# Kernel tuning notes

Hardware: AMD Instinct MI355X
Metric: run time of the kernel (lower is better)

## Reference

```python
import jax, jax.numpy as jnp
import numpy as np
import math

B, T, D, K, KER, H = 2, 2048, 1024, 16, 7, 2048


def _decay_logit_init(k: int, dmin: float = 0.9, dmax: float = 0.999) -> np.ndarray:
    decays = np.exp(np.linspace(math.log(dmin), math.log(dmax), k))
    return (np.log(decays) - np.log1p(-decays)).astype(np.float32)


def setup_inputs() -> dict:
    key = jax.random.key(0)
    ks = jax.random.split(key, 12)
    s = 0.02
    return {
        "x": jax.random.normal(ks[0], (B, T, D), jnp.float32),
        "conv_w": jax.random.normal(ks[1], (D, KER), jnp.float32) * s,   # depthwise causal conv taps
        "gate_w": jax.random.normal(ks[2], (D, D), jnp.float32) * (D ** -0.5),
        "gate_b": jnp.zeros((D,), jnp.float32),
        "up_w": jax.random.normal(ks[3], (D, H), jnp.float32) * (D ** -0.5),
        "up_b": jnp.zeros((H,), jnp.float32),
        "down_w": jax.random.normal(ks[4], (H, D), jnp.float32) * (H ** -0.5),
        "down_b": jnp.zeros((D,), jnp.float32),
        "sin_w": jax.random.normal(ks[5], (D, K * D), jnp.float32) * (D ** -0.5),
        "sout_w": jax.random.normal(ks[6], (K * D, D), jnp.float32) * ((K * D) ** -0.5),
        "decay_logit": jnp.asarray(_decay_logit_init(K)),
        "gl_w": jax.random.normal(ks[7], (D, 1), jnp.float32) * (D ** -0.5),
        "gl_b": jnp.zeros((1,), jnp.float32),
    }


def _rmsnorm(x, eps=1e-6):
    return x * jax.lax.rsqrt(jnp.mean(x * x, axis=-1, keepdims=True) + eps)


def reference(x, conv_w, gate_w, gate_b, up_w, up_b, down_w, down_b,
              sin_w, sout_w, decay_logit, gl_w, gl_b):
    b, t, d = x.shape
    k_taps = conv_w.shape[1]
    nk = decay_logit.shape[0]

    u = _rmsnorm(x)  # (B,T,D)

    # --- local mixer: causal depthwise conv (zero history buffer) + sigmoid gate + SiLU MLP ---
    u_pad = jnp.pad(u, ((0, 0), (k_taps - 1, 0), (0, 0)))
    y = sum(conv_w[:, j] * u_pad[:, j:j + t, :] for j in range(k_taps))  # (B,T,D)
    g = jax.nn.sigmoid(u @ gate_w + gate_b)
    h = y * g
    local = jax.nn.silu(h @ up_w + up_b) @ down_w + down_b

    # --- state bank: K leaky integrators, s_t = a*s_{t-1} + (1-a)*z_t ---
    z = (u @ sin_w).reshape(b, t, nk, d)  # (B,T,K,D)
    a = jax.nn.sigmoid(decay_logit)[:, None]  # (K,1)

    def step(s, z_t):
        s = a * s + (1.0 - a) * z_t
        return s, s

    s0 = jnp.zeros((b, nk, d), x.dtype)
    _, S = jax.lax.scan(step, s0, jnp.swapaxes(z, 0, 1))  # (T,B,K,D)
    S = jnp.swapaxes(S, 0, 1).reshape(b, t, nk * d)
    long_path = S @ sout_w  # (B,T,D)

    # --- gate fusion + residual (memory table is empty at init -> mem term == 0) ---
    g_long = jax.nn.sigmoid(u @ gl_w + gl_b)  # (B,T,1)
    return x + local + g_long * long_path
```

## Files before the change

kernel.cpp:

```cpp
#include <hip/hip_runtime.h>
#include <cstdint>
#include <cstddef>

typedef __attribute__((ext_vector_type(8))) short short8;
typedef __attribute__((ext_vector_type(4))) float floatx4;

#define DEV static __device__ __forceinline__

#define PSTRIDE ((size_t)4096 * 1024)

DEV unsigned short f2bf(float f) {
  union { float f; uint32_t u; } v; v.f = f;
  uint32_t r = v.u + 0x7fffu + ((v.u >> 16) & 1u);
  return (unsigned short)(r >> 16);
}
DEV float bf2f(unsigned short h) {
  union { uint32_t u; float f; } v; v.u = ((uint32_t)h) << 16; return v.f;
}
DEV float sigmoidf_(float x) { return 1.f / (1.f + __expf(-x)); }

DEV void gld_lds16(const unsigned short* g, unsigned short* l) {
  __builtin_amdgcn_global_load_lds(
      (const __attribute__((address_space(1))) void*)g,
      (__attribute__((address_space(3))) void*)l, 16, 0, 0);
}

__global__ __launch_bounds__(256) void transpose_kernel(
    const float* __restrict__ W, unsigned short* __restrict__ Wt,
    int Kdim, int Ndim) {
  __shared__ float tile[32][33];
  const int n0 = blockIdx.x * 32;
  const int k0 = blockIdx.y * 32;
  const int tx = threadIdx.x & 31;
  const int ty = threadIdx.x >> 5;
#pragma unroll
  for (int r = 0; r < 32; r += 8)
    tile[ty + r][tx] = W[(size_t)(k0 + ty + r) * Ndim + n0 + tx];
  __syncthreads();
#pragma unroll
  for (int r = 0; r < 32; r += 8)
    Wt[(size_t)(n0 + ty + r) * Kdim + k0 + tx] = f2bf(tile[tx][ty + r]);
}

__global__ __launch_bounds__(256) void cast_kernel(
    const float* __restrict__ W, unsigned short* __restrict__ Wb) {
  const size_t i = (size_t)blockIdx.x * 256 + threadIdx.x;
  const float4 v = ((const float4*)W)[i];
  ushort4 o;
  o.x = f2bf(v.x); o.y = f2bf(v.y); o.z = f2bf(v.z); o.w = f2bf(v.w);
  ((ushort4*)Wb)[i] = o;
}

__global__ __launch_bounds__(256) void rmsnorm_kernel(
    const float* __restrict__ x, const float* __restrict__ gl_w,
    const float* __restrict__ gl_b, unsigned short* __restrict__ u,
    float* __restrict__ gl_logit) {
  const int row = blockIdx.x;
  const int tid = threadIdx.x;
  const float4 v = ((const float4*)(x + (size_t)row * 1024))[tid];
  float ss = v.x * v.x + v.y * v.y + v.z * v.z + v.w * v.w;
#pragma unroll
  for (int o = 32; o > 0; o >>= 1) ss += __shfl_down(ss, o, 64);
  __shared__ float red[4];
  if ((tid & 63) == 0) red[tid >> 6] = ss;
  __syncthreads();
  const float tot = red[0] + red[1] + red[2] + red[3];
  const float r = rsqrtf(tot * (1.f / 1024.f) + 1e-6f);
  const float ux = v.x * r, uy = v.y * r, uz = v.z * r, uw = v.w * r;
  ushort4 ub;
  ub.x = f2bf(ux); ub.y = f2bf(uy); ub.z = f2bf(uz); ub.w = f2bf(uw);
  ((ushort4*)(u + (size_t)row * 1024))[tid] = ub;
  const float4 w4 = ((const float4*)gl_w)[tid];
  float dot = ux * w4.x + uy * w4.y + uz * w4.z + uw * w4.w;
#pragma unroll
  for (int o = 32; o > 0; o >>= 1) dot += __shfl_down(dot, o, 64);
  __syncthreads();
  if ((tid & 63) == 0) red[tid >> 6] = dot;
  __syncthreads();
  if (tid == 0) gl_logit[row] = red[0] + red[1] + red[2] + red[3] + gl_b[0];
}

template <int EPI>
__global__ __launch_bounds__(256, 2) void gemm_bt(
    const unsigned short* __restrict__ A, const unsigned short* __restrict__ Bt,
    const float* __restrict__ bias, void* __restrict__ Cout, int Ndim, int Kdim) {
  __shared__ unsigned short As[128 * 32];
  __shared__ unsigned short Bs[128 * 32];
  const int tid = threadIdx.x;
  const int wave = tid >> 6;
  const int lane = tid & 63;
  const size_t row0 = (size_t)blockIdx.x * 128;
  const size_t col0 = (size_t)blockIdx.y * 128;

  const int srow = wave * 32 + (lane >> 2);
  const int kofs = (lane & 3) * 8;
  const unsigned short* pA0 = A + (row0 + srow) * (size_t)Kdim + kofs;
  const unsigned short* pA1 = A + (row0 + srow + 16) * (size_t)Kdim + kofs;
  const unsigned short* pB0 = Bt + (col0 + srow) * (size_t)Kdim + kofs;
  const unsigned short* pB1 = Bt + (col0 + srow + 16) * (size_t)Kdim + kofs;
  unsigned short* lA0 = &As[(wave * 2 + 0) * 512];
  unsigned short* lA1 = &As[(wave * 2 + 1) * 512];
  unsigned short* lB0 = &Bs[(wave * 2 + 0) * 512];
  unsigned short* lB1 = &Bs[(wave * 2 + 1) * 512];

  const int wm = (wave & 1) * 64;
  const int wn = (wave >> 1) * 64;
  const int lr = lane & 15;
  const int lq = lane >> 4;
  const int a_off = (wm + lr) * 32 + lq * 8;
  const int b_off = (wn + lr) * 32 + lq * 8;

  floatx4 acc[4][4];
#pragma unroll
  for (int i = 0; i < 4; i++)
#pragma unroll
    for (int j = 0; j < 4; j++) acc[i][j] = floatx4{0.f, 0.f, 0.f, 0.f};

  for (int kt = 0; kt < Kdim; kt += 32) {
    __syncthreads();
    gld_lds16(pA0, lA0);
    gld_lds16(pA1, lA1);
    gld_lds16(pB0, lB0);
    gld_lds16(pB1, lB1);
    pA0 += 32; pA1 += 32; pB0 += 32; pB1 += 32;
    __syncthreads();
    short8 af[4], bfr[4];
#pragma unroll
    for (int i = 0; i < 4; i++) af[i] = *(const short8*)&As[a_off + i * 16 * 32];
#pragma unroll
    for (int j = 0; j < 4; j++) bfr[j] = *(const short8*)&Bs[b_off + j * 16 * 32];
#pragma unroll
    for (int i = 0; i < 4; i++)
#pragma unroll
      for (int j = 0; j < 4; j++)
        acc[i][j] = __builtin_amdgcn_mfma_f32_16x16x32_bf16(af[i], bfr[j], acc[i][j], 0, 0, 0);
  }

#pragma unroll
  for (int i = 0; i < 4; i++) {
    const size_t rbase = row0 + wm + 16 * i + lq * 4;
#pragma unroll
    for (int j = 0; j < 4; j++) {
      const size_t c = col0 + wn + 16 * j + lr;
#pragma unroll
      for (int r = 0; r < 4; r++) {
        float v = acc[i][j][r];
        const size_t off = (rbase + r) * (size_t)Ndim + c;
        if constexpr (EPI == 2) {
          v += bias[c];
          ((unsigned short*)Cout)[off] = f2bf(v * sigmoidf_(v));
        } else {
          ((unsigned short*)Cout)[off] = f2bf(v);
        }
      }
    }
  }
}

__global__ __launch_bounds__(256, 2) void gemm_splitkP(
    const unsigned short* __restrict__ A, const unsigned short* __restrict__ Bt,
    unsigned short* __restrict__ PBase, int Kdim, int splitLen) {
  __shared__ unsigned short As[128 * 32];
  __shared__ unsigned short Bs[128 * 32];
  const int split = blockIdx.z;
  const int k0 = split * splitLen;
  const int klen = min(splitLen, Kdim - k0);
  const int tid = threadIdx.x;
  const int wave = tid >> 6;
  const int lane = tid & 63;
  const size_t row0 = (size_t)blockIdx.x * 128;
  const size_t col0 = (size_t)blockIdx.y * 128;

  const int srow = wave * 32 + (lane >> 2);
  const int kofs = (lane & 3) * 8;
  const unsigned short* pA0 = A + (row0 + srow) * (size_t)Kdim + k0 + kofs;
  const unsigned short* pA1 = A + (row0 + srow + 16) * (size_t)Kdim + k0 + kofs;
  const unsigned short* pB0 = Bt + (col0 + srow) * (size_t)Kdim + k0 + kofs;
  const unsigned short* pB1 = Bt + (col0 + srow + 16) * (size_t)Kdim + k0 + kofs;
  unsigned short* lA0 = &As[(wave * 2 + 0) * 512];
  unsigned short* lA1 = &As[(wave * 2 + 1) * 512];
  unsigned short* lB0 = &Bs[(wave * 2 + 0) * 512];
  unsigned short* lB1 = &Bs[(wave * 2 + 1) * 512];

  const int wm = (wave & 1) * 64;
  const int wn = (wave >> 1) * 64;
  const int lr = lane & 15;
  const int lq = lane >> 4;
  const int a_off = (wm + lr) * 32 + lq * 8;
  const int b_off = (wn + lr) * 32 + lq * 8;

  floatx4 acc[4][4];
#pragma unroll
  for (int i = 0; i < 4; i++)
#pragma unroll
    for (int j = 0; j < 4; j++) acc[i][j] = floatx4{0.f, 0.f, 0.f, 0.f};

  for (int kt = 0; kt < klen; kt += 32) {
    __syncthreads();
    gld_lds16(pA0, lA0);
    gld_lds16(pA1, lA1);
    gld_lds16(pB0, lB0);
    gld_lds16(pB1, lB1);
    pA0 += 32; pA1 += 32; pB0 += 32; pB1 += 32;
    __syncthreads();
    short8 af[4], bfr[4];
#pragma unroll
    for (int i = 0; i < 4; i++) af[i] = *(const short8*)&As[a_off + i * 16 * 32];
#pragma unroll
    for (int j = 0; j < 4; j++) bfr[j] = *(const short8*)&Bs[b_off + j * 16 * 32];
#pragma unroll
    for (int i = 0; i < 4; i++)
#pragma unroll
      for (int j = 0; j < 4; j++)
        acc[i][j] = __builtin_amdgcn_mfma_f32_16x16x32_bf16(af[i], bfr[j], acc[i][j], 0, 0, 0);
  }

  unsigned short* P = PBase + (size_t)split * PSTRIDE;
#pragma unroll
  for (int i = 0; i < 4; i++) {
    const size_t rbase = row0 + wm + 16 * i + lq * 4;
#pragma unroll
    for (int j = 0; j < 4; j++) {
      const size_t c = col0 + wn + 16 * j + lr;
#pragma unroll
      for (int r = 0; r < 4; r++)
        P[(rbase + r) * 1024 + c] = f2bf(acc[i][j][r]);
    }
  }
}

__global__ __launch_bounds__(256, 2) void gemm_mt(
    const unsigned short* __restrict__ OT, const unsigned short* __restrict__ SB,
    unsigned short* __restrict__ MT) {
  __shared__ unsigned short As[128 * 32];
  __shared__ unsigned short Bs[128 * 32];
  const int kb = blockIdx.z;
  const int tid = threadIdx.x;
  const int wave = tid >> 6;
  const int lane = tid & 63;
  const size_t row0 = (size_t)blockIdx.x * 128;
  const size_t col0 = (size_t)blockIdx.y * 128;
  const size_t ld = 16384;

  const int srow = wave * 32 + (lane >> 2);
  const int kofs = (lane & 3) * 8;
  const unsigned short* pA0 = OT + (row0 + srow) * ld + kb * 1024 + kofs;
  const unsigned short* pA1 = OT + (row0 + srow + 16) * ld + kb * 1024 + kofs;
  const unsigned short* pB0 = SB + (col0 + srow) * ld + kb * 1024 + kofs;
  const unsigned short* pB1 = SB + (col0 + srow + 16) * ld + kb * 1024 + kofs;
  unsigned short* lA0 = &As[(wave * 2 + 0) * 512];
  unsigned short* lA1 = &As[(wave * 2 + 1) * 512];
  unsigned short* lB0 = &Bs[(wave * 2 + 0) * 512];
  unsigned short* lB1 = &Bs[(wave * 2 + 1) * 512];

  const int wm = (wave & 1) * 64;
  const int wn = (wave >> 1) * 64;
  const int lr = lane & 15;
  const int lq = lane >> 4;
  const int a_off = (wm + lr) * 32 + lq * 8;
  const int b_off = (wn + lr) * 32 + lq * 8;

  floatx4 acc[4][4];
#pragma unroll
  for (int i = 0; i < 4; i++)
#pragma unroll
    for (int j = 0; j < 4; j++) acc[i][j] = floatx4{0.f, 0.f, 0.f, 0.f};

  for (int kt = 0; kt < 1024; kt += 32) {
    __syncthreads();
    gld_lds16(pA0, lA0);
    gld_lds16(pA1, lA1);
    gld_lds16(pB0, lB0);
    gld_lds16(pB1, lB1);
    pA0 += 32; pA1 += 32; pB0 += 32; pB1 += 32;
    __syncthreads();
    short8 af[4], bfr[4];
#pragma unroll
    for (int i = 0; i < 4; i++) af[i] = *(const short8*)&As[a_off + i * 16 * 32];
#pragma unroll
    for (int j = 0; j < 4; j++) bfr[j] = *(const short8*)&Bs[b_off + j * 16 * 32];
#pragma unroll
    for (int i = 0; i < 4; i++)
#pragma unroll
      for (int j = 0; j < 4; j++)
        acc[i][j] = __builtin_amdgcn_mfma_f32_16x16x32_bf16(af[i], bfr[j], acc[i][j], 0, 0, 0);
  }

#pragma unroll
  for (int i = 0; i < 4; i++) {
    const size_t rbase = row0 + wm + 16 * i + lq * 4;
#pragma unroll
    for (int j = 0; j < 4; j++) {
      const size_t c = col0 + wn + 16 * j + lr;
#pragma unroll
      for (int r = 0; r < 4; r++)
        MT[(rbase + r) * ld + kb * 1024 + c] = f2bf(acc[i][j][r]);
    }
  }
}

__global__ __launch_bounds__(256) void convgate2_kernel(
    const unsigned short* __restrict__ u, const float* __restrict__ conv_w,
    const unsigned short* __restrict__ gp, const float* __restrict__ gate_b,
    unsigned short* __restrict__ h) {
  const size_t idx = (size_t)blockIdx.x * 256 + threadIdx.x;
  const int d = (int)(idx & 1023);
  const int t = (int)((idx >> 10) & 2047);
  const unsigned short* up = u + idx;
  float acc = 0.f;
#pragma unroll
  for (int j = 0; j < 7; ++j) {
    const int tt = t - 6 + j;
    if (tt >= 0) acc += conv_w[d * 7 + j] * bf2f(up[(j - 6) * 1024]);
  }
  const float logit = bf2f(gp[idx]) + bf2f(gp[idx + PSTRIDE]) + gate_b[d];
  h[idx] = f2bf(acc * sigmoidf_(logit));
}

__global__ __launch_bounds__(256) void fold4_kernel(
    const float* __restrict__ x, const unsigned short* __restrict__ dp,
    const float* __restrict__ down_b, float* __restrict__ out) {
  const size_t idx = (size_t)blockIdx.x * 256 + threadIdx.x;
  const float s = bf2f(dp[idx]) + bf2f(dp[idx + PSTRIDE]) +
                  bf2f(dp[idx + 2 * PSTRIDE]) + bf2f(dp[idx + 3 * PSTRIDE]);
  out[idx] = x[idx] + s + down_b[idx & 1023];
}

__global__ __launch_bounds__(256) void reduce3_kernel(
    const unsigned short* __restrict__ p, const float* __restrict__ gl,
    float* __restrict__ out) {
  const size_t idx = (size_t)blockIdx.x * 256 + threadIdx.x;
  const float g = sigmoidf_(gl[idx >> 10]);
  const float s = bf2f(p[idx]) + bf2f(p[idx + PSTRIDE]) + bf2f(p[idx + 2 * PSTRIDE]);
  out[idx] += g * s;
}

__global__ __launch_bounds__(256) void scan1u_kernel(
    const unsigned short* __restrict__ u, const float* __restrict__ decay_logit,
    float* __restrict__ carry) {
  const int gid = blockIdx.x * 256 + threadIdx.x;
  const int d = gid & 1023;
  const int b = (gid >> 10) & 1;
  const int c = gid >> 11;
  float a[16], s[16];
#pragma unroll
  for (int k = 0; k < 16; ++k) { a[k] = sigmoidf_(decay_logit[k]); s[k] = 0.f; }
  const unsigned short* p = u + ((size_t)b * 2048 + c * 128) * 1024 + d;
#pragma unroll 2
  for (int t = 0; t < 128; ++t) {
    const float uv = bf2f(*p);
    p += 1024;
#pragma unroll
    for (int k = 0; k < 16; ++k) s[k] = fmaf(a[k], s[k], (1.f - a[k]) * uv);
  }
#pragma unroll
  for (int k = 0; k < 16; ++k)
    carry[(size_t)((c * 2 + b) * 16 + k) * 1024 + d] = s[k];
}

__global__ __launch_bounds__(256) void scan2u_kernel(
    float* __restrict__ carry, const float* __restrict__ decay_logit) {
  const int gid = blockIdx.x * 256 + threadIdx.x;
  const int d = gid & 1023;
  const int k = (gid >> 10) & 15;
  const int b = gid >> 14;
  const float a = sigmoidf_(decay_logit[k]);
  float aL = a;
#pragma unroll
  for (int i = 0; i < 7; ++i) aL *= aL;
  float s = 0.f;
#pragma unroll
  for (int c = 0; c < 16; ++c) {
    const size_t idx = (size_t)((c * 2 + b) * 16 + k) * 1024 + d;
    const float Lc = carry[idx];
    carry[idx] = s;
    s = fmaf(aL, s, Lc);
  }
}

__global__ __launch_bounds__(256) void scan3u_kernel(
    const unsigned short* __restrict__ u, const float* __restrict__ decay_logit,
    const float* __restrict__ carry, unsigned short* __restrict__ Ucat) {
  const int gid = blockIdx.x * 256 + threadIdx.x;
  const int d = gid & 1023;
  const int k = (gid >> 10) & 15;
  const int b = (gid >> 14) & 1;
  const int c = gid >> 15;
  const float a = sigmoidf_(decay_logit[k]);
  const float na = 1.f - a;
  float s = carry[(size_t)((c * 2 + b) * 16 + k) * 1024 + d];
  const unsigned short* p = u + ((size_t)b * 2048 + c * 128) * 1024 + d;
  unsigned short* q = Ucat + ((size_t)b * 2048 + c * 128) * 16384 + k * 1024 + d;
#pragma unroll 4
  for (int t = 0; t < 128; ++t) {
    s = fmaf(a, s, na * bf2f(*p));
    *q = f2bf(s);
    p += 1024;
    q += 16384;
  }
}

extern "C" void kernel_launch(void* const* d_in, const int* in_sizes, int n_in,
                              void* d_out, int out_size, void* d_ws,
                              size_t ws_size, hipStream_t stream) {
  const float* x      = (const float*)d_in[0];
  const float* conv_w = (const float*)d_in[1];
  const float* gate_w = (const float*)d_in[2];
  const float* gate_b = (const float*)d_in[3];
  const float* up_w   = (const float*)d_in[4];
  const float* up_b   = (const float*)d_in[5];
  const float* down_w = (const float*)d_in[6];
  const float* down_b = (const float*)d_in[7];
  const float* sin_w  = (const float*)d_in[8];
  const float* sout_w = (const float*)d_in[9];
  const float* decay  = (const float*)d_in[10];
  const float* gl_w   = (const float*)d_in[11];
  const float* gl_b   = (const float*)d_in[12];
  float* out = (float*)d_out;
  char* ws = (char*)d_ws;

  auto Ucat = (unsigned short*)(ws + ((size_t)0 << 20));
  auto GWT  = (unsigned short*)(ws + ((size_t)0 << 20));
  auto GP   = (unsigned short*)(ws + ((size_t)2 << 20));
  auto Hb   = (unsigned short*)(ws + ((size_t)18 << 20));
  auto UWT  = (unsigned short*)(ws + ((size_t)26 << 20));
  auto Mb   = (unsigned short*)(ws + ((size_t)30 << 20));
  auto DWT  = (unsigned short*)(ws + ((size_t)46 << 20));
  auto DP   = (unsigned short*)(ws + ((size_t)50 << 20));
  auto SB   = (unsigned short*)(ws + ((size_t)0 << 20));
  auto OT   = (unsigned short*)(ws + ((size_t)32 << 20));
  auto MT   = (unsigned short*)(ws + ((size_t)128 << 20));
  auto U    = (unsigned short*)(ws + ((size_t)160 << 20));
  auto P    = (unsigned short*)(ws + ((size_t)160 << 20));
  auto CARRY= (float*)(ws + ((size_t)168 << 20));
  auto GL   = (float*)(ws + ((size_t)184 << 20));

  rmsnorm_kernel<<<4096, 256, 0, stream>>>(x, gl_w, gl_b, U, GL);

  transpose_kernel<<<dim3(32, 32), 256, 0, stream>>>(gate_w, GWT, 1024, 1024);
  gemm_splitkP<<<dim3(32, 8, 2), 256, 0, stream>>>(U, GWT, GP, 1024, 512);
  convgate2_kernel<<<16384, 256, 0, stream>>>(U, conv_w, GP, gate_b, Hb);
  transpose_kernel<<<dim3(64, 32), 256, 0, stream>>>(up_w, UWT, 1024, 2048);
  gemm_bt<2><<<dim3(32, 16), 256, 0, stream>>>(Hb, UWT, up_b, Mb, 2048, 1024);
  transpose_kernel<<<dim3(32, 64), 256, 0, stream>>>(down_w, DWT, 2048, 1024);
  gemm_splitkP<<<dim3(32, 8, 4), 256, 0, stream>>>(Mb, DWT, DP, 2048, 512);
  fold4_kernel<<<16384, 256, 0, stream>>>(x, DP, down_b, out);

  cast_kernel<<<16384, 256, 0, stream>>>(sin_w, SB);
  transpose_kernel<<<dim3(32, 512), 256, 0, stream>>>(sout_w, OT, 16384, 1024);
  gemm_mt<<<dim3(8, 8, 16), 256, 0, stream>>>(OT, SB, MT);

  scan1u_kernel<<<128, 256, 0, stream>>>(U, decay, CARRY);
  scan2u_kernel<<<128, 256, 0, stream>>>(CARRY, decay);
  scan3u_kernel<<<2048, 256, 0, stream>>>(U, decay, CARRY, Ucat);

  gemm_splitkP<<<dim3(32, 8, 3), 256, 0, stream>>>(Ucat, MT, P, 16384, 5472);
  reduce3_kernel<<<16384, 256, 0, stream>>>(P, GL, out);
}
```

Baseline: 608.2 us.

## Replace split-K GEMMs with 256x256-tile double-buffered pipelined MFMA kernel

Introduces a templated 256x256-tile GEMM with 512 threads, a double-buffered 128KB LDS stage, swizzled LDS offsets, and interleaved global-to-LDS prefetch with MFMA phases using setprio and barriers. It replaces the down-projection split-K GEMM, the sout/sin weight-product GEMM, and the large state-path GEMM, cutting LDS reloads per FLOP. When the workspace is large enough it also uses four K-splits instead of three, with a matching reduction kernel. The larger tiles give fewer blocks, which may underfill the device, and the split count now depends on the workspace size.

```diff
diff --git a/kernel.cpp b/kernel.cpp
--- a/kernel.cpp
+++ b/kernel.cpp
@@ -229,74 +229,123 @@
   }
 }
 
-__global__ __launch_bounds__(256, 2) void gemm_mt(
-    const unsigned short* __restrict__ OT, const unsigned short* __restrict__ SB,
-    unsigned short* __restrict__ MT) {
-  __shared__ unsigned short As[128 * 32];
-  __shared__ unsigned short Bs[128 * 32];
-  const int kb = blockIdx.z;
+template <int MODE>
+__global__ __launch_bounds__(512, 2) void gemm256(
+    const unsigned short* __restrict__ A, const unsigned short* __restrict__ B,
+    unsigned short* __restrict__ Cbase, int splitLen) {
+  __shared__ unsigned short lds[65536];
+  constexpr int LD = (MODE == 2) ? 2048 : 16384;
   const int tid = threadIdx.x;
-  const int wave = tid >> 6;
-  const int lane = tid & 63;
-  const size_t row0 = (size_t)blockIdx.x * 128;
-  const size_t col0 = (size_t)blockIdx.y * 128;
-  const size_t ld = 16384;
-
-  const int srow = wave * 32 + (lane >> 2);
-  const int kofs = (lane & 3) * 8;
-  const unsigned short* pA0 = OT + (row0 + srow) * ld + kb * 1024 + kofs;
-  const unsigned short* pA1 = OT + (row0 + srow + 16) * ld + kb * 1024 + kofs;
-  const unsigned short* pB0 = SB + (col0 + srow) * ld + kb * 1024 + kofs;
-  const unsigned short* pB1 = SB + (col0 + srow + 16) * ld + kb * 1024 + kofs;
-  unsigned short* lA0 = &As[(wave * 2 + 0) * 512];
-  unsigned short* lA1 = &As[(wave * 2 + 1) * 512];
-  unsigned short* lB0 = &Bs[(wave * 2 + 0) * 512];
-  unsigned short* lB1 = &Bs[(wave * 2 + 1) * 512];
-
-  const int wm = (wave & 1) * 64;
-  const int wn = (wave >> 1) * 64;
-  const int lr = lane & 15;
-  const int lq = lane >> 4;
-  const int a_off = (wm + lr) * 32 + lq * 8;
-  const int b_off = (wn + lr) * 32 + lq * 8;
-
-  floatx4 acc[4][4];
-#pragma unroll
-  for (int i = 0; i < 4; i++)
-#pragma unroll
-    for (int j = 0; j < 4; j++) acc[i][j] = floatx4{0.f, 0.f, 0.f, 0.f};
-
-  for (int kt = 0; kt < 1024; kt += 32) {
-    __syncthreads();
-    gld_lds16(pA0, lA0);
-    gld_lds16(pA1, lA1);
-    gld_lds16(pB0, lB0);
-    gld_lds16(pB1, lB1);
-    pA0 += 32; pA1 += 32; pB0 += 32; pB1 += 32;
-    __syncthreads();
-    short8 af[4], bfr[4];
-#pragma unroll
-    for (int i = 0; i < 4; i++) af[i] = *(const short8*)&As[a_off + i * 16 * 32];
-#pragma unroll
-    for (int j = 0; j < 4; j++) bfr[j] = *(const short8*)&Bs[b_off + j * 16 * 32];
-#pragma unroll
-    for (int i = 0; i < 4; i++)
-#pragma unroll
-      for (int j = 0; j < 4; j++)
-        acc[i][j] = __builtin_amdgcn_mfma_f32_16x16x32_bf16(af[i], bfr[j], acc[i][j], 0, 0, 0);
-  }
-
-#pragma unroll
-  for (int i = 0; i < 4; i++) {
-    const size_t rbase = row0 + wm + 16 * i + lq * 4;
-#pragma unroll
-    for (int j = 0; j < 4; j++) {
-      const size_t c = col0 + wn + 16 * j + lr;
-#pragma unroll
-      for (int r = 0; r < 4; r++)
-        MT[(rbase + r) * ld + kb * 1024 + c] = f2bf(acc[i][j][r]);
+  const int w = tid >> 6;
+  const int l = tid & 63;
+  const int wr = w >> 2;
+  const int wc = w & 3;
+  const size_t row0 = (size_t)blockIdx.x * 256;
+  const size_t col0 = (size_t)blockIdx.y * 256;
+  const int z = blockIdx.z;
+  int k0, nkt;
+  if constexpr (MODE == 0) {
+    k0 = z * splitLen;
+    int klen = 16384 - k0; if (klen > splitLen) klen = splitLen;
+    nkt = klen >> 6;
+  } else if constexpr (MODE == 1) {
+    k0 = z << 10; nkt = 16;
+  } else {
+    k0 = z << 9; nkt = 8;
+  }
+
+  const int lp = l ^ (((l >> 5) & 1) << 1);
+  const unsigned short* gA = A + (row0 + w * 16 + (lp >> 3)) * (size_t)LD + k0 + (lp & 7) * 8;
+  const unsigned short* gB = B + (col0 + w * 16 + (lp >> 3)) * (size_t)LD + k0 + (lp & 7) * 8;
+  const int sA = w * 1024;
+  const int sB = 16384 + w * 1024;
+
+  const int lr = l & 15;
+  const int lq = l >> 4;
+  const int lqs = lq ^ (((lr >> 2) & 1) << 1);
+  const int aoff = (wr * 128 + lr) * 64 + lqs * 8;
+  const int boff = 16384 + (wc * 64 + lr) * 64 + lqs * 8;
+
+#define STG_A(bufb, st, h) { \
+    const unsigned short* s_ = gA + (size_t)(h) * (128 * LD) + (size_t)(st) * 64; \
+    unsigned short* d_ = &lds[(bufb) * 32768 + (h) * 8192 + sA]; \
+    gld_lds16(s_, d_); gld_lds16(s_ + 8 * LD, d_ + 512); }
+#define STG_B(bufb, st, h) { \
+    const unsigned short* s_ = gB + (size_t)(h) * (128 * LD) + (size_t)(st) * 64; \
+    unsigned short* d_ = &lds[(bufb) * 32768 + (h) * 8192 + sB]; \
+    gld_lds16(s_, d_); gld_lds16(s_ + 8 * LD, d_ + 512); }
+
+  floatx4 acc[8][4];
+#pragma unroll
+  for (int i = 0; i < 8; ++i)
+#pragma unroll
+    for (int j = 0; j < 4; ++j) acc[i][j] = floatx4{0.f, 0.f, 0.f, 0.f};
+
+  STG_A(0, 0, 0) STG_A(0, 0, 1) STG_B(0, 0, 0) STG_B(0, 0, 1)
+  STG_B(1, 1, 0) STG_B(1, 1, 1)
+  asm volatile("s_waitcnt vmcnt(4)" ::: "memory");
+  __builtin_amdgcn_s_barrier();
+
+  short8 bfr[4][2];
+
+#define MM2(MI, NJ) \
+  acc[MI][NJ] = __builtin_amdgcn_mfma_f32_16x16x32_bf16(af_[(MI) & 1][0], bfr[NJ][0], acc[MI][NJ], 0, 0, 0); \
+  acc[MI][NJ] = __builtin_amdgcn_mfma_f32_16x16x32_bf16(af_[(MI) & 1][1], bfr[NJ][1], acc[MI][NJ], 0, 0, 0);
+
+#define PHASE(Q, STAGE_STMT, TAIL) { \
+    short8 af_[2][2]; \
+    af_[0][0] = *(const short8*)&lds[cb + aoff + (Q * 2 + 0) * 1024]; \
+    af_[0][1] = *(const short8*)&lds[cb + aoff + (Q * 2 + 0) * 1024 + 32]; \
+    af_[1][0] = *(const short8*)&lds[cb + aoff + (Q * 2 + 1) * 1024]; \
+    af_[1][1] = *(const short8*)&lds[cb + aoff + (Q * 2 + 1) * 1024 + 32]; \
+    STAGE_STMT \
+    __builtin_amdgcn_s_barrier(); \
+    asm volatile("s_waitcnt lgkmcnt(0)" ::: "memory"); \
+    __builtin_amdgcn_sched_barrier(0); \
+    __builtin_amdgcn_s_setprio(1); \
+    MM2(Q * 2 + 0, 0) MM2(Q * 2 + 0, 1) MM2(Q * 2 + 0, 2) MM2(Q * 2 + 0, 3) \
+    MM2(Q * 2 + 1, 0) MM2(Q * 2 + 1, 1) MM2(Q * 2 + 1, 2) MM2(Q * 2 + 1, 3) \
+    __builtin_amdgcn_s_setprio(0); \
+    TAIL; \
+    __builtin_amdgcn_s_barrier(); }
+
+  for (int S = 0; S < nkt; ++S) {
+    const int cur = S & 1;
+    const int oth = cur ^ 1;
+    const int cb = cur * 32768;
+    const int t1 = (S + 1 < nkt) ? S + 1 : nkt - 1;
+    const int t2 = (S + 2 < nkt) ? S + 2 : nkt - 1;
+#pragma unroll
+    for (int nj = 0; nj < 4; ++nj) {
+      bfr[nj][0] = *(const short8*)&lds[cb + boff + nj * 1024];
+      bfr[nj][1] = *(const short8*)&lds[cb + boff + nj * 1024 + 32];
     }
-  }
+    PHASE(0, STG_A(oth, t1, 0), )
+    PHASE(1, STG_A(oth, t1, 1), )
+    PHASE(2, STG_B(cur, t2, 0), )
+    PHASE(3, STG_B(cur, t2, 1), asm volatile("s_waitcnt vmcnt(4)" ::: "memory"))
+  }
+
+#pragma unroll
+  for (int mi = 0; mi < 8; ++mi) {
+    const size_t r0 = row0 + wr * 128 + mi * 16 + lq * 4;
+#pragma unroll
+    for (int nj = 0; nj < 4; ++nj) {
+      const size_t c = col0 + wc * 64 + nj * 16 + lr;
+#pragma unroll
+      for (int r = 0; r < 4; ++r) {
+        const float v = acc[mi][nj][r];
+        if constexpr (MODE == 1)
+          Cbase[(r0 + r) * 16384 + ((size_t)z << 10) + c] = f2bf(v);
+        else
+          Cbase[(size_t)z * PSTRIDE + (r0 + r) * 1024 + c] = f2bf(v);
+      }
+    }
+  }
+#undef PHASE
+#undef MM2
+#undef STG_A
+#undef STG_B
 }
 
 __global__ __launch_bounds__(256) void convgate2_kernel(
@@ -326,12 +375,15 @@
   out[idx] = x[idx] + s + down_b[idx & 1023];
 }
 
-__global__ __launch_bounds__(256) void reduce3_kernel(
+template <int NS>
+__global__ __launch_bounds__(256) void reduceNg_kernel(
     const unsigned short* __restrict__ p, const float* __restrict__ gl,
     float* __restrict__ out) {
   const size_t idx = (size_t)blockIdx.x * 256 + threadIdx.x;
   const float g = sigmoidf_(gl[idx >> 10]);
-  const float s = bf2f(p[idx]) + bf2f(p[idx + PSTRIDE]) + bf2f(p[idx + 2 * PSTRIDE]);
+  float s = 0.f;
+#pragma unroll
+  for (int i = 0; i < NS; ++i) s += bf2f(p[idx + (size_t)i * PSTRIDE]);
   out[idx] += g * s;
 }
 
@@ -419,6 +471,8 @@
   float* out = (float*)d_out;
   char* ws = (char*)d_ws;
 
+  const bool big = ws_size >= (((size_t)192 << 20) + ((size_t)1 << 16));
+
   auto Ucat = (unsigned short*)(ws + ((size_t)0 << 20));
   auto GWT  = (unsigned short*)(ws + ((size_t)0 << 20));
   auto GP   = (unsigned short*)(ws + ((size_t)2 << 20));
@@ -433,7 +487,7 @@
   auto U    = (unsigned short*)(ws + ((size_t)160 << 20));
   auto P    = (unsigned short*)(ws + ((size_t)160 << 20));
   auto CARRY= (float*)(ws + ((size_t)168 << 20));
-  auto GL   = (float*)(ws + ((size_t)184 << 20));
+  auto GL   = (float*)(ws + (big ? ((size_t)192 << 20) : ((size_t)184 << 20)));
 
   rmsnorm_kernel<<<4096, 256, 0, stream>>>(x, gl_w, gl_b, U, GL);
 
@@ -443,17 +497,22 @@
   transpose_kernel<<<dim3(64, 32), 256, 0, stream>>>(up_w, UWT, 1024, 2048);
   gemm_bt<2><<<dim3(32, 16), 256, 0, stream>>>(Hb, UWT, up_b, Mb, 2048, 1024);
   transpose_kernel<<<dim3(32, 64), 256, 0, stream>>>(down_w, DWT, 2048, 1024);
-  gemm_splitkP<<<dim3(32, 8, 4), 256, 0, stream>>>(Mb, DWT, DP, 2048, 512);
+  gemm256<2><<<dim3(16, 4, 4), 512, 0, stream>>>(Mb, DWT, DP, 512);
   fold4_kernel<<<16384, 256, 0, stream>>>(x, DP, down_b, out);
 
   cast_kernel<<<16384, 256, 0, stream>>>(sin_w, SB);
   transpose_kernel<<<dim3(32, 512), 256, 0, stream>>>(sout_w, OT, 16384, 1024);
-  gemm_mt<<<dim3(8, 8, 16), 256, 0, stream>>>(OT, SB, MT);
+  gemm256<1><<<dim3(4, 4, 16), 512, 0, stream>>>(OT, SB, MT, 1024);
 
   scan1u_kernel<<<128, 256, 0, stream>>>(U, decay, CARRY);
   scan2u_kernel<<<128, 256, 0, stream>>>(CARRY, decay);
   scan3u_kernel<<<2048, 256, 0, stream>>>(U, decay, CARRY, Ucat);
 
-  gemm_splitkP<<<dim3(32, 8, 3), 256, 0, stream>>>(Ucat, MT, P, 16384, 5472);
-  reduce3_kernel<<<16384, 256, 0, stream>>>(P, GL, out);
-}
+  if (big) {
+    gemm256<0><<<dim3(16, 4, 4), 512, 0, stream>>>(Ucat, MT, P, 4096);
+    reduceNg_kernel<4><<<16384, 256, 0, stream>>>(P, GL, out);
+  } else {
+    gemm256<0><<<dim3(16, 4, 3), 512, 0, stream>>>(Ucat, MT, P, 5504);
+    reduceNg_kernel<3><<<16384, 256, 0, stream>>>(P, GL, out);
+  }
+}
```

Measured after the change: 537.1 us. 1.13x faster.
